# Performance work log

Hardware: AMD Instinct MI355X
Metric: run time of the kernel (lower is better)

## Reference

```python
import jax, jax.numpy as jnp
import numpy as np

N_HOS, N_TYP, N_STRUCTS = 2, 3, 8
N_COMBOS = N_HOS * N_TYP  # 6
BATCH = 32768
N_ITERS = 150  # PDHG iterations to solve the per-sample QP

S_NP = np.array([[1,0,0,1,0,1,0,0],
                 [0,1,0,1,0,0,1,0],
                 [0,0,1,0,1,0,0,1],
                 [1,0,0,0,1,1,0,0],
                 [0,1,0,0,0,0,1,1],
                 [0,0,1,1,1,0,0,0]], dtype=np.float32)


def setup_inputs() -> dict:
    key = jax.random.key(0)
    ks = jax.random.split(key, 10)
    def lin(kw, fan_in, fan_out):
        lim = 1.0 / np.sqrt(fan_in)
        kw1, kw2 = jax.random.split(kw)
        W = jax.random.uniform(kw1, (fan_out, fan_in), jnp.float32, -lim, lim)
        b = jax.random.uniform(kw2, (fan_out,), jnp.float32, -lim, lim)
        return W, b
    W1, b1 = lin(ks[0], 6, 20)
    W2, b2 = lin(ks[1], 20, 20)
    W3, b3 = lin(ks[2], 20, 20)
    W4, b4 = lin(ks[3], 20, 8)
    X = jax.random.uniform(ks[4], (BATCH, N_HOS, N_TYP), jnp.float32)  # nonneg bids -> feasible QP (x=0)
    return {"X": X, "W1": W1, "b1": b1, "W2": W2, "b2": b2, "W3": W3, "b3": b3,
            "W4": W4, "b4": b4, "S": jnp.asarray(S_NP), "batch_size": BATCH}


def _solve_qp(z, b, S):
    """Batched PDHG for: max w.x - ||x-z||_2  s.t. x>=0, S x <= b, with w = 1.
    z: [B, ns], b: [B, m], S: [m, ns]. Returns x: [B, ns]."""
    B, ns = z.shape
    m = S.shape[0]
    w = jnp.ones_like(z)
    # K = [S; -I]; Frobenius bound on spectral norm (safe step sizes)
    L = jnp.sqrt(jnp.sum(S * S) + ns)
    tau = 0.9 / L
    sigma = 0.9 / L

    def prox_f(u):
        # prox of tau*(||x-z|| - w.x) at u  (closed form: shifted norm shrinkage)
        v = u + tau * w - z
        nv = jnp.linalg.norm(v, axis=-1, keepdims=True)
        scale = jnp.maximum(1.0 - tau / jnp.maximum(nv, 1e-12), 0.0)
        return z + scale * v

    def step(carry, _):
        x, l1, l2 = carry
        x_new = prox_f(x - tau * (l1 @ S - l2))  # K^T lam = S^T l1 - l2
        xbar = 2.0 * x_new - x
        l1n = jnp.maximum(l1 + sigma * (xbar @ S.T) - sigma * b, 0.0)  # dual of Sx<=b
        l2n = jnp.maximum(l2 - sigma * xbar, 0.0)                      # dual of -x<=0
        return (x_new, l1n, l2n), None

    x0 = jnp.maximum(z, 0.0)
    l1 = jnp.zeros((B, m), z.dtype)
    l2 = jnp.zeros((B, ns), z.dtype)
    (x, _, _), _ = jax.lax.scan(step, (x0, l1, l2), None, length=N_ITERS)
    return x


def reference(X, W1, b1, W2, b2, W3, b3, W4, b4, S, batch_size):
    B = X.shape[0]
    Z = X.reshape(B, -1)                       # [B, 6] = bids flattened (also the QP rhs b)
    h = jnp.tanh(Z @ W1.T + b1)
    h = jnp.tanh(h @ W2.T + b2)
    h = jnp.tanh(h @ W3.T + b3)
    z = jnp.tanh(h @ W4.T + b4)                # [B, 8] anchor point for QP
    return _solve_qp(z, Z, S)                  # [B, 8] allocation
```

## Files before the change

kernel.cpp:

```cpp
#include <hip/hip_runtime.h>
#include <math.h>


#define NITERS 150

__device__ __forceinline__ float ftanh(float a) {
    float e = __expf(2.0f * a);
    return fmaf(-2.0f, __builtin_amdgcn_rcpf(e + 1.0f), 1.0f);
}

#define FOR20(M) M(0) M(1) M(2) M(3) M(4) M(5) M(6) M(7) M(8) M(9) \
                 M(10) M(11) M(12) M(13) M(14) M(15) M(16) M(17) M(18) M(19)
#define FOR8(M)  M(0) M(1) M(2) M(3) M(4) M(5) M(6) M(7)
#define FOR6(M)  M(0) M(1) M(2) M(3) M(4) M(5)

#define DOT20(W, base, H) \
  ( (fmaf(W[(base)+0],H##0,  fmaf(W[(base)+1],H##1,  fmaf(W[(base)+2],H##2,  fmaf(W[(base)+3],H##3,  W[(base)+4]*H##4)))) \
   + fmaf(W[(base)+5],H##5,  fmaf(W[(base)+6],H##6,  fmaf(W[(base)+7],H##7,  fmaf(W[(base)+8],H##8,  W[(base)+9]*H##9))))) \
  + (fmaf(W[(base)+10],H##10, fmaf(W[(base)+11],H##11, fmaf(W[(base)+12],H##12, fmaf(W[(base)+13],H##13, W[(base)+14]*H##14)))) \
   + fmaf(W[(base)+15],H##15, fmaf(W[(base)+16],H##16, fmaf(W[(base)+17],H##17, fmaf(W[(base)+18],H##18, W[(base)+19]*H##19))))) )

#define DOT6(W, base, P) \
  ( fmaf(W[(base)+0],P##0, fmaf(W[(base)+1],P##1, W[(base)+2]*P##2)) \
  + fmaf(W[(base)+3],P##3, fmaf(W[(base)+4],P##4, W[(base)+5]*P##5)) )

__global__ __launch_bounds__(64)
__attribute__((amdgpu_waves_per_eu(1, 1), amdgpu_flat_work_group_size(64, 64)))
void matchnet_kernel(
    const float* __restrict__ X,
    const float* __restrict__ W1, const float* __restrict__ b1,
    const float* __restrict__ W2, const float* __restrict__ b2,
    const float* __restrict__ W3, const float* __restrict__ b3,
    const float* __restrict__ W4, const float* __restrict__ b4,
    float* __restrict__ out, int B)
{
    const int gid = blockIdx.x * 64 + threadIdx.x;
    if (gid >= B) return;

    const float TAU = 0.9f / sqrtf(26.0f);
    const float SIG = TAU;
    const float TS  = TAU * SIG;

    float zin0, zin1, zin2, zin3, zin4, zin5;
    {
        const float2* xp = (const float2*)(X + (size_t)gid * 6);
        float2 p0 = xp[0], p1 = xp[1], p2 = xp[2];
        zin0 = p0.x; zin1 = p0.y; zin2 = p1.x;
        zin3 = p1.y; zin4 = p2.x; zin5 = p2.y;
    }

#define L1ROW(j) float h1_##j = ftanh(b1[j] + DOT6(W1, (j)*6, zin));
    FOR20(L1ROW)
#define L2ROW(j) float h2_##j = ftanh(b2[j] + DOT20(W2, (j)*20, h1_));
    FOR20(L2ROW)
#define L3ROW(j) float h3_##j = ftanh(b3[j] + DOT20(W3, (j)*20, h2_));
    FOR20(L3ROW)
#define ZROW(j)  float z##j  = ftanh(b4[j] + DOT20(W4, (j)*20, h3_));
    FOR8(ZROW)

#define INIT8(j) \
    float zpt##j = z##j + TAU; \
    float xz##j  = fmaxf(z##j, 0.0f) - z##j + TAU; \
    float q##j   = 0.0f; \
    float p##j   = xz##j;
    FOR8(INIT8)

#define INIT6(i) float l1_##i = 0.0f; float sb##i = SIG * zin##i;
    FOR6(INIT6)

#pragma unroll 1
    for (int it = 0; it < NITERS; ++it) {
        float t03 = l1_0 + l1_3;
        float t14 = l1_1 + l1_4;
        float t25 = l1_2 + l1_5;
        float st3 = (l1_0 + l1_1) + l1_5;
        float st4 = (l1_2 + l1_3) + l1_5;
        float st7 = l1_2 + l1_4;

        float v0 = fmaf(-TAU, t03, p0);
        float v1 = fmaf(-TAU, t14, p1);
        float v2 = fmaf(-TAU, t25, p2);
        float v3 = fmaf(-TAU, st3, p3);
        float v4 = fmaf(-TAU, st4, p4);
        float v5 = fmaf(-TAU, t03, p5);
        float v6 = fmaf(-TAU, t14, p6);
        float v7 = fmaf(-TAU, st7, p7);

#define ZX(j) float zx##j = zpt##j - xz##j;
        FOR8(ZX)

        float n01 = fmaf(v0, v0, v1*v1);
        float n23 = fmaf(v2, v2, v3*v3);
        float n45 = fmaf(v4, v4, v5*v5);
        float n67 = fmaf(v6, v6, v7*v7);
        float nv2 = (n01 + n23) + (n45 + n67);
        float scale = fmaxf(fmaf(-TAU, __builtin_amdgcn_rsqf(nv2), 1.0f), 0.0f);
        float ss2 = scale + scale;

#define UPD8(j) \
        float xb##j = fmaf(ss2, v##j, zx##j); \
        xz##j = fmaf(scale, v##j, TAU); \
        q##j  = fmaxf(fmaf(-TS, xb##j, q##j), 0.0f); \
        p##j  = xz##j + q##j;
        FOR8(UPD8)

        float r0 = (xb0 + xb3) + xb5;
        float r1 = (xb1 + xb3) + xb6;
        float r2 = (xb2 + xb4) + xb7;
        float r3 = (xb0 + xb4) + xb5;
        float r4 = (xb1 + xb6) + xb7;
        float r5 = (xb2 + xb3) + xb4;

#define L1UPD(i) l1_##i = fmaxf(fmaf(SIG, r##i, l1_##i) - sb##i, 0.0f);
        L1UPD(0) L1UPD(1) L1UPD(2) L1UPD(3) L1UPD(4) L1UPD(5)
    }

    float4* op = (float4*)(out + (size_t)gid * 8);
    op[0] = make_float4(xz0 + z0 - TAU, xz1 + z1 - TAU,
                        xz2 + z2 - TAU, xz3 + z3 - TAU);
    op[1] = make_float4(xz4 + z4 - TAU, xz5 + z5 - TAU,
                        xz6 + z6 - TAU, xz7 + z7 - TAU);
}

extern "C" void kernel_launch(void* const* d_in, const int* in_sizes, int n_in,
                              void* d_out, int out_size, void* d_ws, size_t ws_size,
                              hipStream_t stream) {
    const float* X  = (const float*)d_in[0];
    const float* W1 = (const float*)d_in[1];
    const float* b1 = (const float*)d_in[2];
    const float* W2 = (const float*)d_in[3];
    const float* b2 = (const float*)d_in[4];
    const float* W3 = (const float*)d_in[5];
    const float* b3 = (const float*)d_in[6];
    const float* W4 = (const float*)d_in[7];
    const float* b4 = (const float*)d_in[8];
    float* out = (float*)d_out;
    const int B = in_sizes[0] / 6;
    const int blocks = (B + 63) / 64;
    hipLaunchKernelGGL(matchnet_kernel, dim3(blocks), dim3(64), 0, stream,
                       X, W1, b1, W2, b2, W3, b3, W4, b4, out, B);
}
```

Baseline: 116.5 us.

## Split each QP sample across 8 lanes using cross-lane permutes for PDHG

Each sample now runs on 8 lanes, one per structure variable, instead of one thread per sample. The S and S^T products go through ds_bpermute gathers, and the norm reduction goes through DPP adds. The launch is 8x wider, with 256-thread blocks and a launch_bounds occupancy hint. The aim is more parallelism and higher occupancy for the serial 150-iteration loop. In exchange, every lane recomputes the whole MLP redundantly, which is 8x duplicate tanh work, and each iteration adds six LDS-permute round trips.

```diff
diff --git a/kernel.cpp b/kernel.cpp
--- a/kernel.cpp
+++ b/kernel.cpp
@@ -9,10 +9,21 @@
     return fmaf(-2.0f, __builtin_amdgcn_rcpf(e + 1.0f), 1.0f);
 }
 
+template<int CTRL>
+__device__ __forceinline__ float dpp_add(float x) {
+    int xi = __builtin_bit_cast(int, x);
+    int yi = __builtin_amdgcn_update_dpp(0, xi, CTRL, 0xF, 0xF, true);
+    return x + __builtin_bit_cast(float, yi);
+}
+
+__device__ __forceinline__ float bperm(int addr, float v) {
+    return __builtin_bit_cast(float,
+        __builtin_amdgcn_ds_bpermute(addr, __builtin_bit_cast(int, v)));
+}
+
 #define FOR20(M) M(0) M(1) M(2) M(3) M(4) M(5) M(6) M(7) M(8) M(9) \
                  M(10) M(11) M(12) M(13) M(14) M(15) M(16) M(17) M(18) M(19)
 #define FOR8(M)  M(0) M(1) M(2) M(3) M(4) M(5) M(6) M(7)
-#define FOR6(M)  M(0) M(1) M(2) M(3) M(4) M(5)
 
 #define DOT20(W, base, H) \
   ( (fmaf(W[(base)+0],H##0,  fmaf(W[(base)+1],H##1,  fmaf(W[(base)+2],H##2,  fmaf(W[(base)+3],H##3,  W[(base)+4]*H##4)))) \
@@ -24,8 +35,7 @@
   ( fmaf(W[(base)+0],P##0, fmaf(W[(base)+1],P##1, W[(base)+2]*P##2)) \
   + fmaf(W[(base)+3],P##3, fmaf(W[(base)+4],P##4, W[(base)+5]*P##5)) )
 
-__global__ __launch_bounds__(64)
-__attribute__((amdgpu_waves_per_eu(1, 1), amdgpu_flat_work_group_size(64, 64)))
+__global__ __launch_bounds__(256, 4)
 void matchnet_kernel(
     const float* __restrict__ X,
     const float* __restrict__ W1, const float* __restrict__ b1,
@@ -34,8 +44,10 @@
     const float* __restrict__ W4, const float* __restrict__ b4,
     float* __restrict__ out, int B)
 {
-    const int gid = blockIdx.x * 64 + threadIdx.x;
-    if (gid >= B) return;
+    const int tid = blockIdx.x * 256 + threadIdx.x;
+    const int s   = tid >> 3;
+    if (s >= B) return;
+    const int g   = tid & 7;
 
     const float TAU = 0.9f / sqrtf(26.0f);
     const float SIG = TAU;
@@ -43,7 +55,7 @@
 
     float zin0, zin1, zin2, zin3, zin4, zin5;
     {
-        const float2* xp = (const float2*)(X + (size_t)gid * 6);
+        const float2* xp = (const float2*)(X + (size_t)s * 6);
         float2 p0 = xp[0], p1 = xp[1], p2 = xp[2];
         zin0 = p0.x; zin1 = p0.y; zin2 = p1.x;
         zin3 = p1.y; zin4 = p2.x; zin5 = p2.y;
@@ -58,68 +70,69 @@
 #define ZROW(j)  float z##j  = ftanh(b4[j] + DOT20(W4, (j)*20, h3_));
     FOR8(ZROW)
 
-#define INIT8(j) \
-    float zpt##j = z##j + TAU; \
-    float xz##j  = fmaxf(z##j, 0.0f) - z##j + TAU; \
-    float q##j   = 0.0f; \
-    float p##j   = xz##j;
-    FOR8(INIT8)
+    const bool gb0 = (g & 1), gb1 = (g & 2), gb2 = (g & 4);
+    float z01 = gb0 ? z1 : z0;
+    float z23 = gb0 ? z3 : z2;
+    float z45 = gb0 ? z5 : z4;
+    float z67 = gb0 ? z7 : z6;
+    float z03 = gb1 ? z23 : z01;
+    float z47 = gb1 ? z67 : z45;
+    float zg  = gb2 ? z47 : z03;
 
-#define INIT6(i) float l1_##i = 0.0f; float sb##i = SIG * zin##i;
-    FOR6(INIT6)
+    float i01 = gb0 ? zin1 : zin0;
+    float i23 = gb0 ? zin3 : zin2;
+    float i45 = gb0 ? zin5 : zin4;
+    float i03 = gb1 ? i23 : i01;
+    float ig  = gb2 ? i45 : i03;
+
+    float zpt = zg + TAU;
+    float xz  = fmaxf(zg, 0.0f) - zg + TAU;
+    float q   = 0.0f;
+    float p   = xz;
+    float l1  = 0.0f;
+    float sb  = SIG * ig;
+
+    const int wl  = threadIdx.x & 63;
+    const int gbase = wl & 56;
+    const int nib = g * 4;
+    const int aStA = (gbase + ((0x21020210u >> nib) & 7)) << 2;
+    const int aStB = (gbase + ((0x44331543u >> nib) & 7)) << 2;
+    const int aStC = (gbase + ((0x00055000u >> nib) & 7)) << 2;
+    const int aRA  = (gbase + ((0x00210210u >> nib) & 7)) << 2;
+    const int aRB  = (gbase + ((0x00364433u >> nib) & 7)) << 2;
+    const int aRC  = (gbase + ((0x00475765u >> nib) & 7)) << 2;
+    const float cm = (g == 3 || g == 4) ? 1.0f : 0.0f;
 
 #pragma unroll 1
     for (int it = 0; it < NITERS; ++it) {
-        float t03 = l1_0 + l1_3;
-        float t14 = l1_1 + l1_4;
-        float t25 = l1_2 + l1_5;
-        float st3 = (l1_0 + l1_1) + l1_5;
-        float st4 = (l1_2 + l1_3) + l1_5;
-        float st7 = l1_2 + l1_4;
+        float s1 = bperm(aStA, l1);
+        float s2 = bperm(aStB, l1);
+        float s3 = bperm(aStC, l1);
+        float st = fmaf(cm, s3, s1 + s2);
 
-        float v0 = fmaf(-TAU, t03, p0);
-        float v1 = fmaf(-TAU, t14, p1);
-        float v2 = fmaf(-TAU, t25, p2);
-        float v3 = fmaf(-TAU, st3, p3);
-        float v4 = fmaf(-TAU, st4, p4);
-        float v5 = fmaf(-TAU, t03, p5);
-        float v6 = fmaf(-TAU, t14, p6);
-        float v7 = fmaf(-TAU, st7, p7);
+        float v = fmaf(-TAU, st, p);
 
-#define ZX(j) float zx##j = zpt##j - xz##j;
-        FOR8(ZX)
+        float nv = v * v;
+        nv = dpp_add<0xB1>(nv);
+        nv = dpp_add<0x4E>(nv);
+        nv = dpp_add<0x141>(nv);
 
-        float n01 = fmaf(v0, v0, v1*v1);
-        float n23 = fmaf(v2, v2, v3*v3);
-        float n45 = fmaf(v4, v4, v5*v5);
-        float n67 = fmaf(v6, v6, v7*v7);
-        float nv2 = (n01 + n23) + (n45 + n67);
-        float scale = fmaxf(fmaf(-TAU, __builtin_amdgcn_rsqf(nv2), 1.0f), 0.0f);
-        float ss2 = scale + scale;
+        float scale = fmaxf(fmaf(-TAU, __builtin_amdgcn_rsqf(nv), 1.0f), 0.0f);
 
-#define UPD8(j) \
-        float xb##j = fmaf(ss2, v##j, zx##j); \
-        xz##j = fmaf(scale, v##j, TAU); \
-        q##j  = fmaxf(fmaf(-TS, xb##j, q##j), 0.0f); \
-        p##j  = xz##j + q##j;
-        FOR8(UPD8)
+        float xb = fmaf(scale + scale, v, zpt - xz);
+        xz = fmaf(scale, v, TAU);
+        q  = fmaxf(fmaf(-TS, xb, q), 0.0f);
+        p  = xz + q;
 
-        float r0 = (xb0 + xb3) + xb5;
-        float r1 = (xb1 + xb3) + xb6;
-        float r2 = (xb2 + xb4) + xb7;
-        float r3 = (xb0 + xb4) + xb5;
-        float r4 = (xb1 + xb6) + xb7;
-        float r5 = (xb2 + xb3) + xb4;
+        float r1 = bperm(aRA, xb);
+        float r2 = bperm(aRB, xb);
+        float r3 = bperm(aRC, xb);
+        float r  = (r1 + r2) + r3;
 
-#define L1UPD(i) l1_##i = fmaxf(fmaf(SIG, r##i, l1_##i) - sb##i, 0.0f);
-        L1UPD(0) L1UPD(1) L1UPD(2) L1UPD(3) L1UPD(4) L1UPD(5)
+        l1 = fmaxf(fmaf(SIG, r, l1) - sb, 0.0f);
     }
 
-    float4* op = (float4*)(out + (size_t)gid * 8);
-    op[0] = make_float4(xz0 + z0 - TAU, xz1 + z1 - TAU,
-                        xz2 + z2 - TAU, xz3 + z3 - TAU);
-    op[1] = make_float4(xz4 + z4 - TAU, xz5 + z5 - TAU,
-                        xz6 + z6 - TAU, xz7 + z7 - TAU);
+    out[tid] = xz + zg - TAU;
 }
 
 extern "C" void kernel_launch(void* const* d_in, const int* in_sizes, int n_in,
@@ -136,7 +149,8 @@
     const float* b4 = (const float*)d_in[8];
     float* out = (float*)d_out;
     const int B = in_sizes[0] / 6;
-    const int blocks = (B + 63) / 64;
-    hipLaunchKernelGGL(matchnet_kernel, dim3(blocks), dim3(64), 0, stream,
+    const int threads = B * 8;
+    const int blocks = (threads + 255) / 256;
+    hipLaunchKernelGGL(matchnet_kernel, dim3(blocks), dim3(256), 0, stream,
                        X, W1, b1, W2, b2, W3, b3, W4, b4, out, B);
 }
```

After: 131.5 us. 1.13x slower.
